# Kernel optimization log

Measured on AMD Instinct MI355X. Metric: run time of the kernel, lower is better.

The kernel has to match this reference:

```python
import jax, jax.numpy as jnp
import numpy as np

N = 1024      # number of atoms
L = 64        # latent_size
VOCAB = 20    # vocab_size (len(ATOM_CATEGORIES))


def _lin(key, fan_in, fan_out):
    # mimic torch nn.Linear init: U(-1/sqrt(fan_in), 1/sqrt(fan_in))
    kw, kb = jax.random.split(key)
    s = 1.0 / np.sqrt(fan_in)
    W = jax.random.uniform(kw, (fan_in, fan_out), minval=-s, maxval=s, dtype=jnp.float32)
    b = jax.random.uniform(kb, (fan_out,), minval=-s, maxval=s, dtype=jnp.float32)
    return W, b


def setup_inputs() -> dict:
    key = jax.random.key(0)
    ks = jax.random.split(key, 9)
    We1, be1 = _lin(ks[3], 2 * L + 1, L)   # mlp_e layer 1
    We2, be2 = _lin(ks[4], L, L)           # mlp_e layer 2
    Wh1, bh1 = _lin(ks[5], L + 1, L)       # mlp_h layer 1
    Wh2, bh2 = _lin(ks[6], L, L)           # mlp_h layer 2
    Wo, bo = _lin(ks[7], L, 1)             # output_mlp
    return {
        "atom_categories": jax.random.randint(ks[0], (N,), 0, VOCAB),
        "atom_coordinates": jax.random.normal(ks[1], (N, 3), dtype=jnp.float32),
        "learnable_matrix": jax.random.normal(ks[2], (VOCAB, L), dtype=jnp.float32),
        "We1": We1, "be1": be1, "We2": We2, "be2": be2,
        "Wh1": Wh1, "bh1": bh1, "Wh2": Wh2, "bh2": bh2,
        "Wo": Wo, "bo": bo,
    }


def reference(atom_categories, atom_coordinates, learnable_matrix,
              We1, be1, We2, be2, Wh1, bh1, Wh2, bh2, Wo, bo):
    Z = atom_coordinates
    # init_H: learnable_matrix.T @ one_hot(cat) == row gather
    H = learnable_matrix[atom_categories]                       # [N, L]

    # pairwise squared distances ||Z_i - Z_j||^2
    d2 = jnp.sum((Z[:, None, :] - Z[None, :, :]) ** 2, axis=-1)  # [N, N]

    # mlp_e layer 1 on concat(H_i, H_j, d2): split We1 to avoid materializing concat
    W1i, W1j, w1z = We1[:L], We1[L:2 * L], We1[2 * L]            # [L,L],[L,L],[L]
    pre_i = H @ W1i                                              # [N, L]
    pre_j = H @ W1j                                              # [N, L]
    h1 = jnp.tanh(pre_i[:, None, :] + pre_j[None, :, :]
                  + d2[:, :, None] * w1z + be1)                  # [N, N, L]
    W_e = jnp.tanh(h1 @ We2 + be2)                               # [N, N, L]

    # V[i] = sum over j != i of sum_l W_e[i,j,l]
    total = jnp.sum(W_e, axis=(1, 2))                            # [N]
    diag = jnp.einsum('iil->i', W_e)                             # [N]
    V = total - diag                                             # [N]

    # mlp_h on concat(H_i, V_i): split Wh1
    hh = jnp.tanh(H @ Wh1[:L] + V[:, None] * Wh1[L] + bh1)       # [N, L]
    newH = jnp.tanh(hh @ Wh2 + bh2)                              # [N, L]

    Hsum = jnp.sum(newH, axis=0)                                 # [L]
    return (Hsum @ Wo + bo)[0]                                   # scalar
```

## Files before the change

kernel.cpp:

```cpp
#include <hip/hip_runtime.h>
#include <hip/hip_bf16.h>


#define N_ATOMS 1024
#define L_DIM 64
#define TPB 256

typedef _Float16 f16x8 __attribute__((ext_vector_type(8)));
typedef float f32x4 __attribute__((ext_vector_type(4)));

__device__ __forceinline__ float tanh_fast(float x) {
    float e = __builtin_amdgcn_exp2f(x * 2.8853900817779268f);
    float r = __builtin_amdgcn_rcpf(e + 1.0f);
    return fmaf(-2.0f, r, 1.0f);
}

__global__ __launch_bounds__(256) void k_prep(const int* __restrict__ cat,
                                              const float* __restrict__ LM,
                                              const float* __restrict__ We1,
                                              const float* __restrict__ be1,
                                              float* __restrict__ H,
                                              float* __restrict__ preI,
                                              float* __restrict__ P3) {
    int t = threadIdx.x;
    int sub = t >> 6, l = t & 63;
    int i = blockIdx.x * 4 + sub;
    __shared__ float hrow[4][L_DIM];
    float hv = LM[cat[i] * L_DIM + l];
    hrow[sub][l] = hv;
    H[i * L_DIM + l] = hv;
    __syncthreads();
    float s1 = 0.f, s2 = 0.f;
#pragma unroll
    for (int m = 0; m < L_DIM; m++) {
        float h = hrow[sub][m];
        s1 = fmaf(h, We1[m * L_DIM + l], s1);
        s2 = fmaf(h, We1[(L_DIM + m) * L_DIM + l], s2);
    }
    preI[i * L_DIM + l] = s1;
    int cc = i >> 4;
    int Ll = i & 15;
    int quad = (l >> 3) & 3;
    int L = quad * 16 + Ll;
    int g = ((l >> 5) << 1) | ((l >> 2) & 1);
    int e2 = l & 3;
    P3[cc * 1024 + g * 256 + L * 4 + e2] = s2 + be1[l];
}

__global__ __launch_bounds__(TPB) void k_pairs(const float* __restrict__ Z,
                                               const float* __restrict__ We1,
                                               const float* __restrict__ We2,
                                               const float* __restrict__ be2,
                                               const float* __restrict__ preI,
                                               const float* __restrict__ P3,
                                               float* __restrict__ V) {
    int i = blockIdx.x;
    int t = threadIdx.x;
    int lane = t & 63;
    int wave = t >> 6;
    int nlo = lane & 15;
    int quad = lane >> 4;

    __shared__ float d2s[N_ATOMS];
    __shared__ float red[TPB];

    float zi0 = Z[i * 3], zi1 = Z[i * 3 + 1], zi2 = Z[i * 3 + 2];
    for (int p = t; p < N_ATOMS; p += TPB) {
        float a = zi0 - Z[p * 3], b = zi1 - Z[p * 3 + 1], c = zi2 - Z[p * 3 + 2];
        d2s[p] = a * a + b * b + c * c;
    }

    f32x4 aiR[4], wzR[4];
#pragma unroll
    for (int g = 0; g < 4; g++) {
        int mb = ((g >> 1) << 5) + (quad << 3) + ((g & 1) << 2);
        aiR[g] = *(const f32x4*)(preI + i * L_DIM + mb);
        wzR[g] = *(const f32x4*)(We1 + 2 * L_DIM * L_DIM + mb);
    }
    float be2R[4];
#pragma unroll
    for (int nt = 0; nt < 4; nt++) be2R[nt] = be2[nt * 16 + nlo];

    f16x8 bH[4][2], bL[4][2];
#pragma unroll
    for (int nt = 0; nt < 4; nt++)
#pragma unroll
        for (int kt = 0; kt < 2; kt++)
#pragma unroll
            for (int e = 0; e < 8; e++) {
                float w = We2[(kt * 32 + quad * 8 + e) * L_DIM + nt * 16 + nlo];
                _Float16 hi = (_Float16)w;
                bH[nt][kt][e] = hi;
                bL[nt][kt][e] = (_Float16)(w - (float)hi);
            }
    __syncthreads();

    float Vacc = 0.f;
    const float* Pbase = P3 + wave * 16 * 1024 + lane * 4;

    f32x4 p0 = *(const f32x4*)(Pbase + 0 * 256);
    f32x4 p1 = *(const f32x4*)(Pbase + 1 * 256);
    f32x4 p2 = *(const f32x4*)(Pbase + 2 * 256);
    f32x4 p3 = *(const f32x4*)(Pbase + 3 * 256);

    for (int k = 0; k < 16; k++) {
        int j0 = (wave * 16 + k) * 16;
        float d2 = d2s[j0 + nlo];

        f16x8 aH[2], aL[2];
#pragma unroll
        for (int e2 = 0; e2 < 4; e2++) {
            {
                float h = tanh_fast(fmaf(d2, wzR[0][e2], aiR[0][e2] + p0[e2]));
                _Float16 hi = (_Float16)h;
                aH[0][e2] = hi; aL[0][e2] = (_Float16)(h - (float)hi);
            }
            {
                float h = tanh_fast(fmaf(d2, wzR[1][e2], aiR[1][e2] + p1[e2]));
                _Float16 hi = (_Float16)h;
                aH[0][4 + e2] = hi; aL[0][4 + e2] = (_Float16)(h - (float)hi);
            }
            {
                float h = tanh_fast(fmaf(d2, wzR[2][e2], aiR[2][e2] + p2[e2]));
                _Float16 hi = (_Float16)h;
                aH[1][e2] = hi; aL[1][e2] = (_Float16)(h - (float)hi);
            }
            {
                float h = tanh_fast(fmaf(d2, wzR[3][e2], aiR[3][e2] + p3[e2]));
                _Float16 hi = (_Float16)h;
                aH[1][4 + e2] = hi; aL[1][4 + e2] = (_Float16)(h - (float)hi);
            }
        }

        if (k < 15) {
            const float* nb = Pbase + (k + 1) * 1024;
            p0 = *(const f32x4*)(nb + 0 * 256);
            p1 = *(const f32x4*)(nb + 1 * 256);
            p2 = *(const f32x4*)(nb + 2 * 256);
            p3 = *(const f32x4*)(nb + 3 * 256);
        }

#pragma unroll
        for (int nt = 0; nt < 4; nt++) {
            f32x4 acc = {0.f, 0.f, 0.f, 0.f};
#pragma unroll
            for (int kt = 0; kt < 2; kt++) {
                acc = __builtin_amdgcn_mfma_f32_16x16x32_f16(aH[kt], bH[nt][kt], acc, 0, 0, 0);
                acc = __builtin_amdgcn_mfma_f32_16x16x32_f16(aL[kt], bH[nt][kt], acc, 0, 0, 0);
                acc = __builtin_amdgcn_mfma_f32_16x16x32_f16(aH[kt], bL[nt][kt], acc, 0, 0, 0);
            }
#pragma unroll
            for (int r = 0; r < 4; r++) {
                int jg = j0 + quad * 4 + r;
                float s = tanh_fast(acc[r] + be2R[nt]);
                Vacc += (jg != i) ? s : 0.f;
            }
        }
    }

    red[t] = Vacc;
    __syncthreads();
    if (t < 64) {
        float r = red[t] + red[t + 64] + red[t + 128] + red[t + 192];
#pragma unroll
        for (int o = 32; o > 0; o >>= 1) r += __shfl_down(r, o);
        if (t == 0) V[i] = r;
    }
}

__global__ __launch_bounds__(256) void k_postfin(const float* __restrict__ H,
                                                 const float* __restrict__ V,
                                                 const float* __restrict__ Wh1,
                                                 const float* __restrict__ bh1,
                                                 const float* __restrict__ Wh2,
                                                 const float* __restrict__ bh2,
                                                 const float* __restrict__ Wo,
                                                 const float* __restrict__ bo,
                                                 float* __restrict__ out) {
    int t = threadIdx.x;
    int sub = t >> 6, l = t & 63;
    int i = blockIdx.x * 4 + sub;
    __shared__ float hrow[4][L_DIM];
    __shared__ float hh[4][L_DIM];
    __shared__ float red[256];
    hrow[sub][l] = H[i * L_DIM + l];
    __syncthreads();
    float s = 0.f;
#pragma unroll
    for (int m = 0; m < L_DIM; m++) s = fmaf(hrow[sub][m], Wh1[m * L_DIM + l], s);
    s = fmaf(V[i], Wh1[L_DIM * L_DIM + l], s) + bh1[l];
    hh[sub][l] = tanh_fast(s);
    __syncthreads();
    float s2 = 0.f;
#pragma unroll
    for (int m = 0; m < L_DIM; m++) s2 = fmaf(hh[sub][m], Wh2[m * L_DIM + l], s2);
    float nh = tanh_fast(s2 + bh2[l]);
    red[t] = nh * Wo[l];
    __syncthreads();
    if (t < 64) {
        float r = red[t] + red[t + 64] + red[t + 128] + red[t + 192];
#pragma unroll
        for (int o = 32; o > 0; o >>= 1) r += __shfl_down(r, o);
        if (t == 0) {
            float add = r + (blockIdx.x == 0 ? bo[0] : 0.f);
            atomicAdd(out, add);
        }
    }
}

extern "C" void kernel_launch(void* const* d_in, const int* in_sizes, int n_in,
                              void* d_out, int out_size, void* d_ws, size_t ws_size,
                              hipStream_t stream) {
    const int*   cat = (const int*)  d_in[0];
    const float* Z   = (const float*)d_in[1];
    const float* LM  = (const float*)d_in[2];
    const float* We1 = (const float*)d_in[3];
    const float* be1 = (const float*)d_in[4];
    const float* We2 = (const float*)d_in[5];
    const float* be2 = (const float*)d_in[6];
    const float* Wh1 = (const float*)d_in[7];
    const float* bh1 = (const float*)d_in[8];
    const float* Wh2 = (const float*)d_in[9];
    const float* bh2 = (const float*)d_in[10];
    const float* Wo  = (const float*)d_in[11];
    const float* bo  = (const float*)d_in[12];
    float* out = (float*)d_out;

    float* ws   = (float*)d_ws;
    float* H    = ws;
    float* preI = H    + N_ATOMS * L_DIM;
    float* P3   = preI + N_ATOMS * L_DIM;
    float* V    = P3   + N_ATOMS * L_DIM;

    hipMemsetAsync(out, 0, sizeof(float), stream);
    k_prep<<<N_ATOMS / 4, 256, 0, stream>>>(cat, LM, We1, be1, H, preI, P3);
    k_pairs<<<N_ATOMS, TPB, 0, stream>>>(Z, We1, We2, be2, preI, P3, V);
    k_postfin<<<N_ATOMS / 4, 256, 0, stream>>>(H, V, Wh1, bh1, Wh2, bh2, Wo, bo, out);
}
```

Before: 143.1 us.

## Fuse post-MLP into pair kernel, prescale tanh constants, drop MFMA split term

The post-processing MLP is fused into the pair kernel, and the memset is folded into the prep kernel, so two launches disappear. The tanh scale constant is folded into preI, P3, wz, We2 and be2, which removes a multiply per element. The bias is used as the initial accumulator, and the second tanh is turned into a sum of reciprocals with an affine fixup. The low-part activation split is dropped (3 MFMAs down to 2 per k-tile), and packed RTZ conversions are used, which cuts MFMA and conversion work at some cost in accuracy.

```diff
diff --git a/kernel.cpp b/kernel.cpp
--- a/kernel.cpp
+++ b/kernel.cpp
@@ -5,12 +5,14 @@
 #define N_ATOMS 1024
 #define L_DIM 64
 #define TPB 256
+#define CSCALE 2.8853900817779268f
 
 typedef _Float16 f16x8 __attribute__((ext_vector_type(8)));
+typedef __fp16  fp16x2 __attribute__((ext_vector_type(2)));
 typedef float f32x4 __attribute__((ext_vector_type(4)));
 
 __device__ __forceinline__ float tanh_fast(float x) {
-    float e = __builtin_amdgcn_exp2f(x * 2.8853900817779268f);
+    float e = __builtin_amdgcn_exp2f(x * CSCALE);
     float r = __builtin_amdgcn_rcpf(e + 1.0f);
     return fmaf(-2.0f, r, 1.0f);
 }
@@ -21,10 +23,12 @@
                                               const float* __restrict__ be1,
                                               float* __restrict__ H,
                                               float* __restrict__ preI,
-                                              float* __restrict__ P3) {
+                                              float* __restrict__ P3,
+                                              float* __restrict__ out) {
     int t = threadIdx.x;
     int sub = t >> 6, l = t & 63;
     int i = blockIdx.x * 4 + sub;
+    if (blockIdx.x == 0 && t == 0) out[0] = 0.f;
     __shared__ float hrow[4][L_DIM];
     float hv = LM[cat[i] * L_DIM + l];
     hrow[sub][l] = hv;
@@ -37,23 +41,30 @@
         s1 = fmaf(h, We1[m * L_DIM + l], s1);
         s2 = fmaf(h, We1[(L_DIM + m) * L_DIM + l], s2);
     }
-    preI[i * L_DIM + l] = s1;
+    preI[i * L_DIM + l] = s1 * CSCALE;
     int cc = i >> 4;
     int Ll = i & 15;
     int quad = (l >> 3) & 3;
     int L = quad * 16 + Ll;
     int g = ((l >> 5) << 1) | ((l >> 2) & 1);
     int e2 = l & 3;
-    P3[cc * 1024 + g * 256 + L * 4 + e2] = s2 + be1[l];
-}
-
-__global__ __launch_bounds__(TPB) void k_pairs(const float* __restrict__ Z,
-                                               const float* __restrict__ We1,
-                                               const float* __restrict__ We2,
-                                               const float* __restrict__ be2,
-                                               const float* __restrict__ preI,
-                                               const float* __restrict__ P3,
-                                               float* __restrict__ V) {
+    P3[cc * 1024 + g * 256 + L * 4 + e2] = (s2 + be1[l]) * CSCALE;
+}
+
+__global__ __launch_bounds__(TPB, 6) void k_main(const float* __restrict__ Z,
+                                                 const float* __restrict__ We1,
+                                                 const float* __restrict__ We2,
+                                                 const float* __restrict__ be2,
+                                                 const float* __restrict__ preI,
+                                                 const float* __restrict__ P3,
+                                                 const float* __restrict__ H,
+                                                 const float* __restrict__ Wh1,
+                                                 const float* __restrict__ bh1,
+                                                 const float* __restrict__ Wh2,
+                                                 const float* __restrict__ bh2,
+                                                 const float* __restrict__ Wo,
+                                                 const float* __restrict__ bo,
+                                                 float* __restrict__ out) {
     int i = blockIdx.x;
     int t = threadIdx.x;
     int lane = t & 63;
@@ -63,6 +74,8 @@
 
     __shared__ float d2s[N_ATOMS];
     __shared__ float red[TPB];
+    __shared__ float hrow_s[L_DIM];
+    __shared__ float hh_s[L_DIM];
 
     float zi0 = Z[i * 3], zi1 = Z[i * 3 + 1], zi2 = Z[i * 3 + 2];
     for (int p = t; p < N_ATOMS; p += TPB) {
@@ -75,11 +88,12 @@
     for (int g = 0; g < 4; g++) {
         int mb = ((g >> 1) << 5) + (quad << 3) + ((g & 1) << 2);
         aiR[g] = *(const f32x4*)(preI + i * L_DIM + mb);
-        wzR[g] = *(const f32x4*)(We1 + 2 * L_DIM * L_DIM + mb);
+        f32x4 wz = *(const f32x4*)(We1 + 2 * L_DIM * L_DIM + mb);
+        wzR[g] = wz * CSCALE;
     }
     float be2R[4];
 #pragma unroll
-    for (int nt = 0; nt < 4; nt++) be2R[nt] = be2[nt * 16 + nlo];
+    for (int nt = 0; nt < 4; nt++) be2R[nt] = be2[nt * 16 + nlo] * CSCALE;
 
     f16x8 bH[4][2], bL[4][2];
 #pragma unroll
@@ -88,14 +102,14 @@
         for (int kt = 0; kt < 2; kt++)
 #pragma unroll
             for (int e = 0; e < 8; e++) {
-                float w = We2[(kt * 32 + quad * 8 + e) * L_DIM + nt * 16 + nlo];
+                float w = We2[(kt * 32 + quad * 8 + e) * L_DIM + nt * 16 + nlo] * CSCALE;
                 _Float16 hi = (_Float16)w;
                 bH[nt][kt][e] = hi;
                 bL[nt][kt][e] = (_Float16)(w - (float)hi);
             }
     __syncthreads();
 
-    float Vacc = 0.f;
+    float Vr = 0.f;
     const float* Pbase = P3 + wave * 16 * 1024 + lane * 4;
 
     f32x4 p0 = *(const f32x4*)(Pbase + 0 * 256);
@@ -107,30 +121,44 @@
         int j0 = (wave * 16 + k) * 16;
         float d2 = d2s[j0 + nlo];
 
-        f16x8 aH[2], aL[2];
+        float h[4][4];
 #pragma unroll
         for (int e2 = 0; e2 < 4; e2++) {
             {
-                float h = tanh_fast(fmaf(d2, wzR[0][e2], aiR[0][e2] + p0[e2]));
-                _Float16 hi = (_Float16)h;
-                aH[0][e2] = hi; aL[0][e2] = (_Float16)(h - (float)hi);
-            }
-            {
-                float h = tanh_fast(fmaf(d2, wzR[1][e2], aiR[1][e2] + p1[e2]));
-                _Float16 hi = (_Float16)h;
-                aH[0][4 + e2] = hi; aL[0][4 + e2] = (_Float16)(h - (float)hi);
-            }
-            {
-                float h = tanh_fast(fmaf(d2, wzR[2][e2], aiR[2][e2] + p2[e2]));
-                _Float16 hi = (_Float16)h;
-                aH[1][e2] = hi; aL[1][e2] = (_Float16)(h - (float)hi);
-            }
-            {
-                float h = tanh_fast(fmaf(d2, wzR[3][e2], aiR[3][e2] + p3[e2]));
-                _Float16 hi = (_Float16)h;
-                aH[1][4 + e2] = hi; aL[1][4 + e2] = (_Float16)(h - (float)hi);
+                float z = fmaf(d2, wzR[0][e2], aiR[0][e2] + p0[e2]);
+                float e = __builtin_amdgcn_exp2f(z);
+                float r = __builtin_amdgcn_rcpf(e + 1.0f);
+                h[0][e2] = fmaf(-2.0f, r, 1.0f);
+            }
+            {
+                float z = fmaf(d2, wzR[1][e2], aiR[1][e2] + p1[e2]);
+                float e = __builtin_amdgcn_exp2f(z);
+                float r = __builtin_amdgcn_rcpf(e + 1.0f);
+                h[1][e2] = fmaf(-2.0f, r, 1.0f);
+            }
+            {
+                float z = fmaf(d2, wzR[2][e2], aiR[2][e2] + p2[e2]);
+                float e = __builtin_amdgcn_exp2f(z);
+                float r = __builtin_amdgcn_rcpf(e + 1.0f);
+                h[2][e2] = fmaf(-2.0f, r, 1.0f);
+            }
+            {
+                float z = fmaf(d2, wzR[3][e2], aiR[3][e2] + p3[e2]);
+                float e = __builtin_amdgcn_exp2f(z);
+                float r = __builtin_amdgcn_rcpf(e + 1.0f);
+                h[3][e2] = fmaf(-2.0f, r, 1.0f);
             }
         }
+        union { f16x8 v; fp16x2 h2[4]; } u0, u1;
+        u0.h2[0] = __builtin_amdgcn_cvt_pkrtz(h[0][0], h[0][1]);
+        u0.h2[1] = __builtin_amdgcn_cvt_pkrtz(h[0][2], h[0][3]);
+        u0.h2[2] = __builtin_amdgcn_cvt_pkrtz(h[1][0], h[1][1]);
+        u0.h2[3] = __builtin_amdgcn_cvt_pkrtz(h[1][2], h[1][3]);
+        u1.h2[0] = __builtin_amdgcn_cvt_pkrtz(h[2][0], h[2][1]);
+        u1.h2[1] = __builtin_amdgcn_cvt_pkrtz(h[2][2], h[2][3]);
+        u1.h2[2] = __builtin_amdgcn_cvt_pkrtz(h[3][0], h[3][1]);
+        u1.h2[3] = __builtin_amdgcn_cvt_pkrtz(h[3][2], h[3][3]);
+        f16x8 aH0 = u0.v, aH1 = u1.v;
 
         if (k < 15) {
             const float* nb = Pbase + (k + 1) * 1024;
@@ -142,69 +170,50 @@
 
 #pragma unroll
         for (int nt = 0; nt < 4; nt++) {
-            f32x4 acc = {0.f, 0.f, 0.f, 0.f};
-#pragma unroll
-            for (int kt = 0; kt < 2; kt++) {
-                acc = __builtin_amdgcn_mfma_f32_16x16x32_f16(aH[kt], bH[nt][kt], acc, 0, 0, 0);
-                acc = __builtin_amdgcn_mfma_f32_16x16x32_f16(aL[kt], bH[nt][kt], acc, 0, 0, 0);
-                acc = __builtin_amdgcn_mfma_f32_16x16x32_f16(aH[kt], bL[nt][kt], acc, 0, 0, 0);
-            }
-#pragma unroll
-            for (int r = 0; r < 4; r++) {
-                int jg = j0 + quad * 4 + r;
-                float s = tanh_fast(acc[r] + be2R[nt]);
-                Vacc += (jg != i) ? s : 0.f;
+            f32x4 acc = {be2R[nt], be2R[nt], be2R[nt], be2R[nt]};
+            acc = __builtin_amdgcn_mfma_f32_16x16x32_f16(aH0, bH[nt][0], acc, 0, 0, 0);
+            acc = __builtin_amdgcn_mfma_f32_16x16x32_f16(aH0, bL[nt][0], acc, 0, 0, 0);
+            acc = __builtin_amdgcn_mfma_f32_16x16x32_f16(aH1, bH[nt][1], acc, 0, 0, 0);
+            acc = __builtin_amdgcn_mfma_f32_16x16x32_f16(aH1, bL[nt][1], acc, 0, 0, 0);
+#pragma unroll
+            for (int r4 = 0; r4 < 4; r4++) {
+                int jg = j0 + quad * 4 + r4;
+                float e = __builtin_amdgcn_exp2f(acc[r4]);
+                float rr = __builtin_amdgcn_rcpf(e + 1.0f);
+                Vr += (jg != i) ? rr : 0.f;
             }
         }
     }
 
-    red[t] = Vacc;
-    __syncthreads();
+    red[t] = Vr;
+    __syncthreads();
+
+    float V;
     if (t < 64) {
         float r = red[t] + red[t + 64] + red[t + 128] + red[t + 192];
 #pragma unroll
-        for (int o = 32; o > 0; o >>= 1) r += __shfl_down(r, o);
-        if (t == 0) V[i] = r;
-    }
-}
-
-__global__ __launch_bounds__(256) void k_postfin(const float* __restrict__ H,
-                                                 const float* __restrict__ V,
-                                                 const float* __restrict__ Wh1,
-                                                 const float* __restrict__ bh1,
-                                                 const float* __restrict__ Wh2,
-                                                 const float* __restrict__ bh2,
-                                                 const float* __restrict__ Wo,
-                                                 const float* __restrict__ bo,
-                                                 float* __restrict__ out) {
-    int t = threadIdx.x;
-    int sub = t >> 6, l = t & 63;
-    int i = blockIdx.x * 4 + sub;
-    __shared__ float hrow[4][L_DIM];
-    __shared__ float hh[4][L_DIM];
-    __shared__ float red[256];
-    hrow[sub][l] = H[i * L_DIM + l];
-    __syncthreads();
-    float s = 0.f;
-#pragma unroll
-    for (int m = 0; m < L_DIM; m++) s = fmaf(hrow[sub][m], Wh1[m * L_DIM + l], s);
-    s = fmaf(V[i], Wh1[L_DIM * L_DIM + l], s) + bh1[l];
-    hh[sub][l] = tanh_fast(s);
-    __syncthreads();
-    float s2 = 0.f;
-#pragma unroll
-    for (int m = 0; m < L_DIM; m++) s2 = fmaf(hh[sub][m], Wh2[m * L_DIM + l], s2);
-    float nh = tanh_fast(s2 + bh2[l]);
-    red[t] = nh * Wo[l];
+        for (int o = 32; o > 0; o >>= 1) r += __shfl_xor(r, o);
+        V = fmaf(-2.0f, r, (float)(1023 * L_DIM));
+        hrow_s[t] = H[i * L_DIM + t];
+    }
     __syncthreads();
     if (t < 64) {
-        float r = red[t] + red[t + 64] + red[t + 128] + red[t + 192];
-#pragma unroll
-        for (int o = 32; o > 0; o >>= 1) r += __shfl_down(r, o);
-        if (t == 0) {
-            float add = r + (blockIdx.x == 0 ? bo[0] : 0.f);
-            atomicAdd(out, add);
-        }
+        float s = 0.f;
+#pragma unroll
+        for (int m = 0; m < L_DIM; m++) s = fmaf(hrow_s[m], Wh1[m * L_DIM + t], s);
+        s = fmaf(V, Wh1[L_DIM * L_DIM + t], s) + bh1[t];
+        hh_s[t] = tanh_fast(s);
+    }
+    __syncthreads();
+    if (t < 64) {
+        float s2 = 0.f;
+#pragma unroll
+        for (int m = 0; m < L_DIM; m++) s2 = fmaf(hh_s[m], Wh2[m * L_DIM + t], s2);
+        float nh = tanh_fast(s2 + bh2[t]);
+        float w = nh * Wo[t];
+#pragma unroll
+        for (int o = 32; o > 0; o >>= 1) w += __shfl_down(w, o);
+        if (t == 0) atomicAdd(out, w + (i == 0 ? bo[0] : 0.f));
     }
 }
 
@@ -230,10 +239,8 @@
     float* H    = ws;
     float* preI = H    + N_ATOMS * L_DIM;
     float* P3   = preI + N_ATOMS * L_DIM;
-    float* V    = P3   + N_ATOMS * L_DIM;
-
-    hipMemsetAsync(out, 0, sizeof(float), stream);
-    k_prep<<<N_ATOMS / 4, 256, 0, stream>>>(cat, LM, We1, be1, H, preI, P3);
-    k_pairs<<<N_ATOMS, TPB, 0, stream>>>(Z, We1, We2, be2, preI, P3, V);
-    k_postfin<<<N_ATOMS / 4, 256, 0, stream>>>(H, V, Wh1, bh1, Wh2, bh2, Wo, bo, out);
-}
+
+    k_prep<<<N_ATOMS / 4, 256, 0, stream>>>(cat, LM, We1, be1, H, preI, P3, out);
+    k_main<<<N_ATOMS, TPB, 0, stream>>>(Z, We1, We2, be2, preI, P3, H,
+                                        Wh1, bh1, Wh2, bh2, Wo, bo, out);
+}
```

Result: slower. 264.1 us (+84.6%).
